# Optimization experiments

Hardware: AMD Instinct MI355X
Metric: run time of the kernel (lower is better)

## Reference

```python
import jax, jax.numpy as jnp
import numpy as np

B, T_V, T_A = 128, 64, 128
E_V, E_A = 1024, 512
H, EMB, C = 1024, 512, 512  # C = input_size - embedding_size
IN = EMB + C               # RNN input size = 1024
VOCAB = 20000


def setup_inputs() -> dict:
    key = jax.random.key(0)
    ks = jax.random.split(key, 26)
    s = 0.02
    inp = {
        "input": jax.random.normal(ks[0], (B, 1, EMB), jnp.float32),
        "enc_visual": jax.random.normal(ks[1], (B, T_V, E_V), jnp.float32),
        "enc_audio": jax.random.normal(ks[2], (B, T_A, E_A), jnp.float32),
        "hidden_state": jax.random.normal(ks[3], (1, B, H), jnp.float32),
        "cell_state": jax.random.normal(ks[4], (1, B, H), jnp.float32),
        # visual attention (Bahdanau): W1:[C,H], W2:[C,E_V], W3:[1,C]
        "W_va1": s * jax.random.normal(ks[5], (C, H), jnp.float32),
        "W_va2": s * jax.random.normal(ks[6], (C, E_V), jnp.float32),
        "W_va3": s * jax.random.normal(ks[7], (1, C), jnp.float32),
        "W_venc": s * jax.random.normal(ks[8], (C, E_V), jnp.float32),
        # audio attention
        "W_aa1": s * jax.random.normal(ks[9], (C, H), jnp.float32),
        "W_aa2": s * jax.random.normal(ks[10], (C, E_A), jnp.float32),
        "W_aa3": s * jax.random.normal(ks[11], (1, C), jnp.float32),
        "W_aenc": s * jax.random.normal(ks[12], (C, E_A), jnp.float32),
        # cross-modal context attention (over 2 context vectors)
        "W_ca1": s * jax.random.normal(ks[13], (C, H), jnp.float32),
        "W_ca2": s * jax.random.normal(ks[14], (C, C), jnp.float32),
        "W_ca3": s * jax.random.normal(ks[15], (1, C), jnp.float32),
        # LSTM-style custom RNN cell params
        "W_ih": s * jax.random.normal(ks[16], (4 * H, IN), jnp.float32),
        "W_hh": s * jax.random.normal(ks[17], (4 * H, H), jnp.float32),
        "b_ih": jnp.zeros((4 * H,), jnp.float32),
        "b_hh": jnp.zeros((4 * H,), jnp.float32),
        # output projection
        "W_out": s * jax.random.normal(ks[18], (VOCAB, H), jnp.float32),
        "b_out": jnp.zeros((VOCAB,), jnp.float32),
    }
    return inp


def _attend(h, enc, W1, W2, W3):
    # h: [B,H]; enc: [B,T,E]. Vectorized Bahdanau attention (original loops over T).
    v1 = h @ W1.T                               # [B,C]
    v2 = jnp.einsum('bte,ce->btc', enc, W2)     # [B,T,C]
    scores = jnp.tanh(v1[:, None, :] + v2) @ W3.T  # [B,T,1]
    attn = jax.nn.softmax(scores[..., 0], axis=1)  # [B,T]
    return jnp.einsum('bt,bte->be', attn, enc)     # [B,E]


def reference(input, enc_visual, enc_audio, hidden_state, cell_state,
              W_va1, W_va2, W_va3, W_venc,
              W_aa1, W_aa2, W_aa3, W_aenc,
              W_ca1, W_ca2, W_ca3,
              W_ih, W_hh, b_ih, b_hh, W_out, b_out):
    h0 = hidden_state[0]   # [B,H]
    c0 = cell_state[0]     # [B,H]

    vc = _attend(h0, enc_visual, W_va1, W_va2, W_va3) @ W_venc.T  # [B,C]
    ac = _attend(h0, enc_audio, W_aa1, W_aa2, W_aa3) @ W_aenc.T   # [B,C]
    all_ctx = jnp.stack([vc, ac], axis=1)                         # [B,2,C]
    final_ctx = _attend(h0, all_ctx, W_ca1, W_ca2, W_ca3)         # [B,C]

    x = jnp.concatenate([input[:, 0, :], jnp.tanh(final_ctx)], axis=-1)  # [B,IN]
    gates = x @ W_ih.T + b_ih + h0 @ W_hh.T + b_hh                 # [B,4H]
    i, f, g, o = jnp.split(gates, 4, axis=-1)
    c_new = jax.nn.sigmoid(f) * c0 + jax.nn.sigmoid(i) * jnp.tanh(g)
    h_new = jax.nn.sigmoid(o) * jnp.tanh(c_new)

    logits = h_new @ W_out.T + b_out                               # [B,V]
    return (logits[:, None, :], h_new[None], c_new[None])
```

## Files before the change

kernel.cpp:

```cpp
#include <hip/hip_runtime.h>
#include <hip/hip_bf16.h>
#include <cstddef>

typedef __attribute__((ext_vector_type(8))) short short8;
typedef __attribute__((ext_vector_type(4))) float f32x4;

#define LSTR 40

static __device__ __forceinline__ short8 pack8(float4 f0, float4 f1) {
    union { __hip_bfloat162 h[4]; short8 s; } u;
    u.h[0] = __float22bfloat162_rn(make_float2(f0.x, f0.y));
    u.h[1] = __float22bfloat162_rn(make_float2(f0.z, f0.w));
    u.h[2] = __float22bfloat162_rn(make_float2(f1.x, f1.y));
    u.h[3] = __float22bfloat162_rn(make_float2(f1.z, f1.w));
    return u.s;
}

static __device__ __forceinline__ void sk_body(
    const float* __restrict__ A, int lda,
    const float* __restrict__ W,
    const float* __restrict__ bias, int addbias,
    float* __restrict__ C, int ldc, int N,
    int kbeg, int kend, int n0, int m0)
{
    __shared__ short As[128 * LSTR];
    __shared__ short Ws[64 * LSTR];
    const int tid  = threadIdx.x;
    const int lane = tid & 63;
    const int wave = tid >> 6;
    const int wm = wave * 32;

    f32x4 acc[2][4];
    #pragma unroll
    for (int i = 0; i < 2; ++i)
        #pragma unroll
        for (int j = 0; j < 4; ++j)
            acc[i][j] = (f32x4){0.f, 0.f, 0.f, 0.f};

    const int srow  = tid >> 2;
    const int skoff = (tid & 3) * 8;
    const int frow  = lane & 15;
    const int fkoff = (lane >> 4) * 8;

    for (int k0 = kbeg; k0 < kend; k0 += 32) {
        #pragma unroll
        for (int p = 0; p < 2; ++p) {
            int row = srow + p * 64;
            const float* sa = A + (size_t)(m0 + row) * lda + k0 + skoff;
            *(short8*)(As + row * LSTR + skoff) =
                pack8(*(const float4*)sa, *(const float4*)(sa + 4));
        }
        {
            int n = n0 + srow;
            short8 v = (short8){0,0,0,0,0,0,0,0};
            if (n < N) {
                const float* sw = W + (size_t)n * lda + k0 + skoff;
                v = pack8(*(const float4*)sw, *(const float4*)(sw + 4));
            }
            *(short8*)(Ws + srow * LSTR + skoff) = v;
        }
        __syncthreads();

        short8 af[2], bf[4];
        #pragma unroll
        for (int i = 0; i < 2; ++i)
            af[i] = *(const short8*)(As + (wm + i * 16 + frow) * LSTR + fkoff);
        #pragma unroll
        for (int j = 0; j < 4; ++j)
            bf[j] = *(const short8*)(Ws + (j * 16 + frow) * LSTR + fkoff);
        #pragma unroll
        for (int i = 0; i < 2; ++i)
            #pragma unroll
            for (int j = 0; j < 4; ++j)
                acc[i][j] = __builtin_amdgcn_mfma_f32_16x16x32_bf16(af[i], bf[j], acc[i][j], 0, 0, 0);
        __syncthreads();
    }

    const int cl = lane & 15;
    const int rq = (lane >> 4) * 4;
    #pragma unroll
    for (int j = 0; j < 4; ++j) {
        int gc = n0 + j * 16 + cl;
        if (gc >= N) continue;
        float b = addbias ? bias[gc] : 0.f;
        #pragma unroll
        for (int i = 0; i < 2; ++i) {
            int gr = m0 + wm + i * 16 + rq;
            #pragma unroll
            for (int r = 0; r < 4; ++r)
                atomicAdd(C + (size_t)(gr + r) * ldc + gc, acc[i][j][r] + b);
        }
    }
}

__global__ __launch_bounds__(256) void gemm_sk(
    const float* __restrict__ A, const float* __restrict__ W,
    const float* __restrict__ bias, float* __restrict__ C,
    int N, int K, int kchunk, int ldc)
{
    int kbeg = blockIdx.y * kchunk;
    sk_body(A, K, W, bias, bias != nullptr && blockIdx.y == 0,
            C, ldc, N, kbeg, kbeg + kchunk, blockIdx.x * 64, blockIdx.z * 128);
}

__global__ __launch_bounds__(256) void hproj3_mfma(
    const float* __restrict__ h0,
    const float* __restrict__ Wa, const float* __restrict__ Wb, const float* __restrict__ Wc,
    float* __restrict__ hbase)
{
    int n0g = blockIdx.x * 64;
    int wsel = n0g >> 9;
    const float* W = (wsel == 0) ? Wa : (wsel == 1) ? Wb : Wc;
    float* C = hbase + (size_t)wsel * 128 * 512;
    int kbeg = blockIdx.y * 128;
    sk_body(h0, 1024, W, nullptr, 0, C, 512, 512, kbeg, kbeg + 128, n0g & 511, 0);
}

__global__ __launch_bounds__(256) void ctxproj_mfma(
    const float* __restrict__ attv, const float* __restrict__ Wv,
    const float* __restrict__ atta, const float* __restrict__ Wa,
    float* __restrict__ ctx)
{
    const float* A; const float* W; float* C; int lda, kb, ke;
    if (blockIdx.z == 0) { A = attv; W = Wv; C = ctx;       lda = 1024; kb = blockIdx.y * 128; ke = kb + 128; }
    else                 { A = atta; W = Wa; C = ctx + 512; lda = 512;  kb = blockIdx.y * 64;  ke = kb + 64;  }
    sk_body(A, lda, W, nullptr, 0, C, 1024, 512, kb, ke, blockIdx.x * 64, 0);
}

__global__ __launch_bounds__(256) void gates_mfma(
    const float* __restrict__ xb, const float* __restrict__ W_ih,
    const float* __restrict__ h0, const float* __restrict__ W_hh,
    float* __restrict__ gates)
{
    int pair = blockIdx.y >> 2;
    const float* A = pair ? h0 : xb;
    const float* W = pair ? W_hh : W_ih;
    int kb = (blockIdx.y & 3) * 256;
    sk_body(A, 1024, W, nullptr, 0, gates, 4096, 4096, kb, kb + 256, blockIdx.x * 64, 0);
}

__global__ __launch_bounds__(256) void scores_fused(
    const float* __restrict__ encv, const float* __restrict__ W_va2,
    const float* __restrict__ hv1,  const float* __restrict__ W_va3,
    float* __restrict__ scv,
    const float* __restrict__ enca, const float* __restrict__ W_aa2,
    const float* __restrict__ ha1,  const float* __restrict__ W_aa3,
    float* __restrict__ sca)
{
    __shared__ short As[64 * LSTR];
    __shared__ short Ws[128 * LSTR];

    const float *A, *W, *v1, *W3;
    float* sc;
    int K, tshift, n0, m0;
    int idx = blockIdx.x;
    if (idx < 512) {
        n0 = (idx >> 7) * 128;  m0 = (idx & 127) * 64;
        A = encv; W = W_va2; v1 = hv1; W3 = W_va3; sc = scv;
        K = 1024; tshift = 6;
    } else {
        idx -= 512;
        n0 = (idx >> 8) * 128;  m0 = (idx & 255) * 64;
        A = enca; W = W_aa2; v1 = ha1; W3 = W_aa3; sc = sca;
        K = 512; tshift = 7;
    }

    const int tid  = threadIdx.x;
    const int lane = tid & 63;
    const int wave = tid >> 6;
    const int wm = (wave >> 1) * 32;
    const int wn = (wave & 1) * 64;

    f32x4 acc[2][4];
    #pragma unroll
    for (int i = 0; i < 2; ++i)
        #pragma unroll
        for (int j = 0; j < 4; ++j)
            acc[i][j] = (f32x4){0.f, 0.f, 0.f, 0.f};

    const int srow  = tid >> 2;
    const int skoff = (tid & 3) * 8;
    const int frow  = lane & 15;
    const int fkoff = (lane >> 4) * 8;

    for (int k0 = 0; k0 < K; k0 += 32) {
        {
            const float* sa = A + (size_t)(m0 + srow) * K + k0 + skoff;
            *(short8*)(As + srow * LSTR + skoff) =
                pack8(*(const float4*)sa, *(const float4*)(sa + 4));
        }
        #pragma unroll
        for (int p = 0; p < 2; ++p) {
            int row = srow + p * 64;
            const float* sw = W + (size_t)(n0 + row) * K + k0 + skoff;
            *(short8*)(Ws + row * LSTR + skoff) =
                pack8(*(const float4*)sw, *(const float4*)(sw + 4));
        }
        __syncthreads();

        short8 af[2], bf[4];
        #pragma unroll
        for (int i = 0; i < 2; ++i)
            af[i] = *(const short8*)(As + (wm + i * 16 + frow) * LSTR + fkoff);
        #pragma unroll
        for (int j = 0; j < 4; ++j)
            bf[j] = *(const short8*)(Ws + (wn + j * 16 + frow) * LSTR + fkoff);
        #pragma unroll
        for (int i = 0; i < 2; ++i)
            #pragma unroll
            for (int j = 0; j < 4; ++j)
                acc[i][j] = __builtin_amdgcn_mfma_f32_16x16x32_bf16(af[i], bf[j], acc[i][j], 0, 0, 0);
        __syncthreads();
    }

    const int cl = lane & 15;
    const int rq = (lane >> 4) * 4;
    #pragma unroll
    for (int i = 0; i < 2; ++i) {
        #pragma unroll
        for (int r = 0; r < 4; ++r) {
            int gr = m0 + wm + i * 16 + rq + r;
            const float* v1row = v1 + (size_t)(gr >> tshift) * 512;
            float p = 0.f;
            #pragma unroll
            for (int j = 0; j < 4; ++j) {
                int gc = n0 + wn + j * 16 + cl;
                p += tanhf(v1row[gc] + acc[i][j][r]) * W3[gc];
            }
            p += __shfl_xor(p, 1, 64);
            p += __shfl_xor(p, 2, 64);
            p += __shfl_xor(p, 4, 64);
            p += __shfl_xor(p, 8, 64);
            if (cl == 0) atomicAdd(sc + gr, p);
        }
    }
}

__global__ __launch_bounds__(256) void attend_out2(
    const float* __restrict__ scv, const float* __restrict__ encv, float* __restrict__ attv,
    const float* __restrict__ sca, const float* __restrict__ enca, float* __restrict__ atta)
{
    const float* sc; const float* enc; float* out;
    int T, E, ec;
    if (blockIdx.y < 4) { sc = scv; enc = encv; out = attv; T = 64;  E = 1024; ec = blockIdx.y; }
    else                { sc = sca; enc = enca; out = atta; T = 128; E = 512;  ec = blockIdx.y - 4; }

    __shared__ float ew[128];
    const int b = blockIdx.x, tid = threadIdx.x;
    __shared__ float raw[128];
    if (tid < T) raw[tid] = sc[(size_t)b * T + tid];
    __syncthreads();
    float m = -1e30f;
    for (int t = 0; t < T; ++t) m = fmaxf(m, raw[t]);
    if (tid < T) ew[tid] = __expf(raw[tid] - m);
    __syncthreads();
    float sum = 0.f;
    for (int t = 0; t < T; ++t) sum += ew[t];
    const float inv = 1.f / sum;

    const int e = ec * 256 + tid;
    const float* encb = enc + (size_t)b * T * E + e;
    float acc = 0.f;
    for (int t = 0; t < T; ++t)
        acc += ew[t] * encb[(size_t)t * E];
    out[(size_t)b * E + e] = acc * inv;
}

__global__ __launch_bounds__(256) void cross_kernel(
    const float* __restrict__ hc1, const float* __restrict__ v2c,
    const float* __restrict__ W3, const float* __restrict__ ctx,
    const float* __restrict__ inp, float* __restrict__ x)
{
    const int C = 512;
    __shared__ float red[256];
    __shared__ float aw[2];
    const int b = blockIdx.x, tid = threadIdx.x;

    float p0 = 0.f, p1 = 0.f;
    for (int c = tid; c < C; c += 256) {
        float h = hc1[(size_t)b * C + c], w = W3[c];
        p0 += tanhf(h + v2c[(size_t)(b * 2 + 0) * C + c]) * w;
        p1 += tanhf(h + v2c[(size_t)(b * 2 + 1) * C + c]) * w;
    }
    red[tid] = p0; __syncthreads();
    for (int s = 128; s; s >>= 1) { if (tid < s) red[tid] += red[tid + s]; __syncthreads(); }
    float s0 = red[0];
    __syncthreads();
    red[tid] = p1; __syncthreads();
    for (int s = 128; s; s >>= 1) { if (tid < s) red[tid] += red[tid + s]; __syncthreads(); }
    if (tid == 0) {
        float s1 = red[0];
        float m = fmaxf(s0, s1);
        float e0 = __expf(s0 - m), e1 = __expf(s1 - m);
        float inv = 1.f / (e0 + e1);
        aw[0] = e0 * inv; aw[1] = e1 * inv;
    }
    __syncthreads();
    float a0 = aw[0], a1 = aw[1];
    for (int c = tid; c < C; c += 256) {
        float fc = a0 * ctx[(size_t)(b * 2 + 0) * C + c]
                 + a1 * ctx[(size_t)(b * 2 + 1) * C + c];
        x[(size_t)b * 1024 + 512 + c] = tanhf(fc);
        x[(size_t)b * 1024 + c] = inp[(size_t)b * 512 + c];
    }
}

__global__ __launch_bounds__(256) void lstm_kernel(
    const float* __restrict__ gates, const float* __restrict__ c0,
    const float* __restrict__ b_ih, const float* __restrict__ b_hh,
    float* __restrict__ hout, float* __restrict__ cout)
{
    const int idx = blockIdx.x * 256 + threadIdx.x;
    const int b = idx >> 10, h = idx & 1023;
    const float* g = gates + (size_t)b * 4096;
    float gi = g[h]        + b_ih[h]        + b_hh[h];
    float gf = g[1024 + h] + b_ih[1024 + h] + b_hh[1024 + h];
    float gg = g[2048 + h] + b_ih[2048 + h] + b_hh[2048 + h];
    float go = g[3072 + h] + b_ih[3072 + h] + b_hh[3072 + h];
    float si = 1.f / (1.f + __expf(-gi));
    float sf = 1.f / (1.f + __expf(-gf));
    float so = 1.f / (1.f + __expf(-go));
    float cn = sf * c0[idx] + si * tanhf(gg);
    float hn = so * tanhf(cn);
    cout[idx] = cn;
    hout[idx] = hn;
}

extern "C" void kernel_launch(void* const* d_in, const int* in_sizes, int n_in,
                              void* d_out, int out_size, void* d_ws, size_t ws_size,
                              hipStream_t stream)
{
    const float* inp    = (const float*)d_in[0];
    const float* encv   = (const float*)d_in[1];
    const float* enca   = (const float*)d_in[2];
    const float* h0     = (const float*)d_in[3];
    const float* c0     = (const float*)d_in[4];
    const float* W_va1  = (const float*)d_in[5];
    const float* W_va2  = (const float*)d_in[6];
    const float* W_va3  = (const float*)d_in[7];
    const float* W_venc = (const float*)d_in[8];
    const float* W_aa1  = (const float*)d_in[9];
    const float* W_aa2  = (const float*)d_in[10];
    const float* W_aa3  = (const float*)d_in[11];
    const float* W_aenc = (const float*)d_in[12];
    const float* W_ca1  = (const float*)d_in[13];
    const float* W_ca2  = (const float*)d_in[14];
    const float* W_ca3  = (const float*)d_in[15];
    const float* W_ih   = (const float*)d_in[16];
    const float* W_hh   = (const float*)d_in[17];
    const float* b_ih   = (const float*)d_in[18];
    const float* b_hh   = (const float*)d_in[19];
    const float* W_out  = (const float*)d_in[20];
    const float* b_out  = (const float*)d_in[21];
    float* out = (float*)d_out;

    float* ws = (float*)d_ws;
    float* hv1  = ws;  ws += 128 * 512;
    float* ha1  = ws;  ws += 128 * 512;
    float* hc1  = ws;  ws += 128 * 512;
    float* scv  = ws;  ws += 128 * 64;
    float* sca  = ws;  ws += 128 * 128;
    float* ctx  = ws;  ws += 128 * 2 * 512;
    float* v2c  = ws;  ws += 128 * 2 * 512;
    float* gates= ws;  ws += (size_t)128 * 4096;
    size_t zero_floats = (size_t)(ws - (float*)d_ws);
    float* xb   = ws;  ws += 128 * 1024;
    float* attv = ws;  ws += 128 * 1024;
    float* atta = ws;  ws += 128 * 512;

    dim3 blk(256);

    hipMemsetAsync(d_ws, 0, zero_floats * sizeof(float), stream);
    hipMemsetAsync(out, 0, (size_t)128 * 20000 * sizeof(float), stream);

    hproj3_mfma<<<dim3(24, 8), blk, 0, stream>>>(h0, W_va1, W_aa1, W_ca1, hv1);
    scores_fused<<<dim3(1536), blk, 0, stream>>>(encv, W_va2, hv1, W_va3, scv,
                                                 enca, W_aa2, ha1, W_aa3, sca);
    attend_out2<<<dim3(128, 6), blk, 0, stream>>>(scv, encv, attv, sca, enca, atta);
    ctxproj_mfma<<<dim3(8, 8, 2), blk, 0, stream>>>(attv, W_venc, atta, W_aenc, ctx);
    gemm_sk<<<dim3(8, 4, 2), blk, 0, stream>>>(ctx, W_ca2, nullptr, v2c, 512, 512, 128, 512);
    cross_kernel<<<128, blk, 0, stream>>>(hc1, v2c, W_ca3, ctx, inp, xb);
    gates_mfma<<<dim3(64, 8), blk, 0, stream>>>(xb, W_ih, h0, W_hh, gates);
    float* hout = out + 2560000;
    float* cout = out + 2560000 + 131072;
    lstm_kernel<<<512, blk, 0, stream>>>(gates, c0, b_ih, b_hh, hout, cout);
    gemm_sk<<<dim3(313, 2, 1), blk, 0, stream>>>(hout, W_out, b_out, out, 20000, 1024, 512, 20000);
}
```

Baseline: 398.5 us.

## Enlarge scores GEMM tile to 128x128, prefetch globals, swizzle LDS

The fused attention-score GEMM now uses 128x128 tiles instead of 64x128, which halves the block count and doubles per-wave MFMA work for more operand reuse. Global loads for the next K-slice go into registers while the current slice is computed, so global latency overlaps with compute. The padded LDS layout is replaced by an XOR-swizzled 32-wide layout meant to avoid bank conflicts without padding. The cost is higher register pressure (more accumulators plus prefetch buffers) and fewer blocks, which may lower occupancy.

```diff
diff --git a/kernel.cpp b/kernel.cpp
--- a/kernel.cpp
+++ b/kernel.cpp
@@ -147,20 +147,20 @@
     const float* __restrict__ ha1,  const float* __restrict__ W_aa3,
     float* __restrict__ sca)
 {
-    __shared__ short As[64 * LSTR];
-    __shared__ short Ws[128 * LSTR];
+    __shared__ short As[128 * 32];
+    __shared__ short Ws[128 * 32];
 
     const float *A, *W, *v1, *W3;
     float* sc;
     int K, tshift, n0, m0;
     int idx = blockIdx.x;
-    if (idx < 512) {
-        n0 = (idx >> 7) * 128;  m0 = (idx & 127) * 64;
+    if (idx < 256) {
+        n0 = (idx >> 6) * 128;  m0 = (idx & 63) * 128;
         A = encv; W = W_va2; v1 = hv1; W3 = W_va3; sc = scv;
         K = 1024; tshift = 6;
     } else {
-        idx -= 512;
-        n0 = (idx >> 8) * 128;  m0 = (idx & 255) * 64;
+        idx -= 256;
+        n0 = (idx >> 7) * 128;  m0 = (idx & 127) * 128;
         A = enca; W = W_aa2; v1 = ha1; W3 = W_aa3; sc = sca;
         K = 512; tshift = 7;
     }
@@ -168,45 +168,63 @@
     const int tid  = threadIdx.x;
     const int lane = tid & 63;
     const int wave = tid >> 6;
-    const int wm = (wave >> 1) * 32;
+    const int wm = (wave >> 1) * 64;
     const int wn = (wave & 1) * 64;
 
-    f32x4 acc[2][4];
+    f32x4 acc[4][4];
     #pragma unroll
-    for (int i = 0; i < 2; ++i)
+    for (int i = 0; i < 4; ++i)
         #pragma unroll
         for (int j = 0; j < 4; ++j)
             acc[i][j] = (f32x4){0.f, 0.f, 0.f, 0.f};
 
-    const int srow  = tid >> 2;
-    const int skoff = (tid & 3) * 8;
+    const int srow = tid >> 1;
+    const int skh  = tid & 1;
+    const float* ga = A + (size_t)(m0 + srow) * K + skh * 16;
+    const float* gw = W + (size_t)(n0 + srow) * K + skh * 16;
+    const int fs = (srow >> 1) & 3;
+    short* wa0 = As + srow * 32 + (((skh * 2)     ^ fs) * 8);
+    short* wa1 = As + srow * 32 + (((skh * 2 + 1) ^ fs) * 8);
+    short* ww0 = Ws + srow * 32 + (((skh * 2)     ^ fs) * 8);
+    short* ww1 = Ws + srow * 32 + (((skh * 2 + 1) ^ fs) * 8);
+
     const int frow  = lane & 15;
-    const int fkoff = (lane >> 4) * 8;
+    const int hi    = lane >> 4;
+    const int fslot = (hi ^ ((frow >> 1) & 3)) * 8;
+    const short* ra = As + (wm + frow) * 32 + fslot;
+    const short* rb = Ws + (wn + frow) * 32 + fslot;
+
+    float4 pa[4], pw[4];
+    #pragma unroll
+    for (int q = 0; q < 4; ++q) {
+        pa[q] = *(const float4*)(ga + q * 4);
+        pw[q] = *(const float4*)(gw + q * 4);
+    }
 
     for (int k0 = 0; k0 < K; k0 += 32) {
-        {
-            const float* sa = A + (size_t)(m0 + srow) * K + k0 + skoff;
-            *(short8*)(As + srow * LSTR + skoff) =
-                pack8(*(const float4*)sa, *(const float4*)(sa + 4));
+        *(short8*)wa0 = pack8(pa[0], pa[1]);
+        *(short8*)wa1 = pack8(pa[2], pa[3]);
+        *(short8*)ww0 = pack8(pw[0], pw[1]);
+        *(short8*)ww1 = pack8(pw[2], pw[3]);
+        __syncthreads();
+
+        if (k0 + 32 < K) {
+            #pragma unroll
+            for (int q = 0; q < 4; ++q) {
+                pa[q] = *(const float4*)(ga + k0 + 32 + q * 4);
+                pw[q] = *(const float4*)(gw + k0 + 32 + q * 4);
+            }
         }
-        #pragma unroll
-        for (int p = 0; p < 2; ++p) {
-            int row = srow + p * 64;
-            const float* sw = W + (size_t)(n0 + row) * K + k0 + skoff;
-            *(short8*)(Ws + row * LSTR + skoff) =
-                pack8(*(const float4*)sw, *(const float4*)(sw + 4));
-        }
-        __syncthreads();
-
-        short8 af[2], bf[4];
-        #pragma unroll
-        for (int i = 0; i < 2; ++i)
-            af[i] = *(const short8*)(As + (wm + i * 16 + frow) * LSTR + fkoff);
+
+        short8 af[4], bf[4];
+        #pragma unroll
+        for (int i = 0; i < 4; ++i)
+            af[i] = *(const short8*)(ra + i * 512);
         #pragma unroll
         for (int j = 0; j < 4; ++j)
-            bf[j] = *(const short8*)(Ws + (wn + j * 16 + frow) * LSTR + fkoff);
-        #pragma unroll
-        for (int i = 0; i < 2; ++i)
+            bf[j] = *(const short8*)(rb + j * 512);
+        #pragma unroll
+        for (int i = 0; i < 4; ++i)
             #pragma unroll
             for (int j = 0; j < 4; ++j)
                 acc[i][j] = __builtin_amdgcn_mfma_f32_16x16x32_bf16(af[i], bf[j], acc[i][j], 0, 0, 0);
@@ -214,9 +232,9 @@
     }
 
     const int cl = lane & 15;
-    const int rq = (lane >> 4) * 4;
+    const int rq = hi * 4;
     #pragma unroll
-    for (int i = 0; i < 2; ++i) {
+    for (int i = 0; i < 4; ++i) {
         #pragma unroll
         for (int r = 0; r < 4; ++r) {
             int gr = m0 + wm + i * 16 + rq + r;
@@ -374,8 +392,8 @@
     hipMemsetAsync(out, 0, (size_t)128 * 20000 * sizeof(float), stream);
 
     hproj3_mfma<<<dim3(24, 8), blk, 0, stream>>>(h0, W_va1, W_aa1, W_ca1, hv1);
-    scores_fused<<<dim3(1536), blk, 0, stream>>>(encv, W_va2, hv1, W_va3, scv,
-                                                 enca, W_aa2, ha1, W_aa3, sca);
+    scores_fused<<<dim3(768), blk, 0, stream>>>(encv, W_va2, hv1, W_va3, scv,
+                                                enca, W_aa2, ha1, W_aa3, sca);
     attend_out2<<<dim3(128, 6), blk, 0, stream>>>(scv, encv, attv, sca, enca, atta);
     ctxproj_mfma<<<dim3(8, 8, 2), blk, 0, stream>>>(attv, W_venc, atta, W_aenc, ctx);
     gemm_sk<<<dim3(8, 4, 2), blk, 0, stream>>>(ctx, W_ca2, nullptr, v2c, 512, 512, 128, 512);
```

Result: slower. 412.7 us (+3.6%).

## Double-buffer LDS tiles with register prefetch and XOR-swizzled layout in GEMMs

Applied to the files above, without the earlier changes.

Both the split-K GEMM body and the fused attention-score GEMM now prefetch the next K-slice from global memory into registers while the current slice is consumed from LDS. They use two LDS buffers so the trailing barrier can be dropped. The padded LDS stride is replaced by an unpadded 32-element row with an XOR swizzle, meant to avoid bank conflicts without wasting space. This targets global-load latency stalls and one barrier per iteration, at the cost of doubled LDS use and more live registers.

```diff
diff --git a/kernel.cpp b/kernel.cpp
--- a/kernel.cpp
+++ b/kernel.cpp
@@ -4,8 +4,6 @@
 
 typedef __attribute__((ext_vector_type(8))) short short8;
 typedef __attribute__((ext_vector_type(4))) float f32x4;
-
-#define LSTR 40
 
 static __device__ __forceinline__ short8 pack8(float4 f0, float4 f1) {
     union { __hip_bfloat162 h[4]; short8 s; } u;
@@ -23,8 +21,8 @@
     float* __restrict__ C, int ldc, int N,
     int kbeg, int kend, int n0, int m0)
 {
-    __shared__ short As[128 * LSTR];
-    __shared__ short Ws[64 * LSTR];
+    __shared__ short As[2][128 * 32];
+    __shared__ short Ws[2][64 * 32];
     const int tid  = threadIdx.x;
     const int lane = tid & 63;
     const int wave = tid >> 6;
@@ -37,47 +35,64 @@
         for (int j = 0; j < 4; ++j)
             acc[i][j] = (f32x4){0.f, 0.f, 0.f, 0.f};
 
-    const int srow  = tid >> 2;
-    const int skoff = (tid & 3) * 8;
-    const int frow  = lane & 15;
-    const int fkoff = (lane >> 4) * 8;
-
-    for (int k0 = kbeg; k0 < kend; k0 += 32) {
-        #pragma unroll
-        for (int p = 0; p < 2; ++p) {
-            int row = srow + p * 64;
-            const float* sa = A + (size_t)(m0 + row) * lda + k0 + skoff;
-            *(short8*)(As + row * LSTR + skoff) =
-                pack8(*(const float4*)sa, *(const float4*)(sa + 4));
-        }
-        {
-            int n = n0 + srow;
-            short8 v = (short8){0,0,0,0,0,0,0,0};
-            if (n < N) {
-                const float* sw = W + (size_t)n * lda + k0 + skoff;
-                v = pack8(*(const float4*)sw, *(const float4*)(sw + 4));
+    const int arow = tid >> 1;
+    const int ah   = tid & 1;
+    const int afs  = (arow >> 1) & 3;
+    const float* gA = A + (size_t)(m0 + arow) * lda + kbeg + ah * 16;
+    const int aoff0 = arow * 32 + (((ah * 2)     ^ afs) * 8);
+    const int aoff1 = arow * 32 + (((ah * 2 + 1) ^ afs) * 8);
+
+    const int wrow  = tid >> 2;
+    const int wslot = tid & 3;
+    const int wvalid = (n0 + wrow) < N;
+    const float* gW = W + (size_t)(n0 + wrow) * lda + kbeg + wslot * 8;
+    const int woff = wrow * 32 + ((wslot ^ ((wrow >> 1) & 3)) * 8);
+
+    const int frow = lane & 15;
+    const int hi   = lane >> 4;
+    const int fsl  = (hi ^ ((frow >> 1) & 3)) * 8;
+    const int ra   = (wm + frow) * 32 + fsl;
+    const int rb   = frow * 32 + fsl;
+
+    float4 pa0, pa1, pa2, pa3, pw0, pw1;
+    pa0 = *(const float4*)(gA);      pa1 = *(const float4*)(gA + 4);
+    pa2 = *(const float4*)(gA + 8);  pa3 = *(const float4*)(gA + 12);
+    if (wvalid) { pw0 = *(const float4*)(gW); pw1 = *(const float4*)(gW + 4); }
+    else        { pw0 = make_float4(0,0,0,0); pw1 = make_float4(0,0,0,0); }
+
+    const int nsteps = (kend - kbeg) >> 5;
+    for (int s = 0; s < nsteps; ++s) {
+        short* as = As[s & 1];
+        short* ws = Ws[s & 1];
+        *(short8*)(as + aoff0) = pack8(pa0, pa1);
+        *(short8*)(as + aoff1) = pack8(pa2, pa3);
+        *(short8*)(ws + woff)  = pack8(pw0, pw1);
+        if (s + 1 < nsteps) {
+            const float* nA = gA + (s + 1) * 32;
+            pa0 = *(const float4*)(nA);      pa1 = *(const float4*)(nA + 4);
+            pa2 = *(const float4*)(nA + 8);  pa3 = *(const float4*)(nA + 12);
+            if (wvalid) {
+                const float* nW = gW + (s + 1) * 32;
+                pw0 = *(const float4*)(nW); pw1 = *(const float4*)(nW + 4);
             }
-            *(short8*)(Ws + srow * LSTR + skoff) = v;
         }
         __syncthreads();
-
         short8 af[2], bf[4];
         #pragma unroll
         for (int i = 0; i < 2; ++i)
-            af[i] = *(const short8*)(As + (wm + i * 16 + frow) * LSTR + fkoff);
+            af[i] = *(const short8*)(as + ra + i * 512);
         #pragma unroll
         for (int j = 0; j < 4; ++j)
-            bf[j] = *(const short8*)(Ws + (j * 16 + frow) * LSTR + fkoff);
+            bf[j] = *(const short8*)(ws + rb + j * 512);
         #pragma unroll
         for (int i = 0; i < 2; ++i)
             #pragma unroll
             for (int j = 0; j < 4; ++j)
                 acc[i][j] = __builtin_amdgcn_mfma_f32_16x16x32_bf16(af[i], bf[j], acc[i][j], 0, 0, 0);
-        __syncthreads();
     }
 
     const int cl = lane & 15;
-    const int rq = (lane >> 4) * 4;
+    const int rq = hi * 4;
     #pragma unroll
     for (int j = 0; j < 4; ++j) {
         int gc = n0 + j * 16 + cl;
@@ -147,8 +162,8 @@
     const float* __restrict__ ha1,  const float* __restrict__ W_aa3,
     float* __restrict__ sca)
 {
-    __shared__ short As[64 * LSTR];
-    __shared__ short Ws[128 * LSTR];
+    __shared__ short As[2][64 * 32];
+    __shared__ short Ws[2][128 * 32];
 
     const float *A, *W, *v1, *W3;
     float* sc;
@@ -178,43 +193,60 @@
         for (int j = 0; j < 4; ++j)
             acc[i][j] = (f32x4){0.f, 0.f, 0.f, 0.f};
 
-    const int srow  = tid >> 2;
-    const int skoff = (tid & 3) * 8;
-    const int frow  = lane & 15;
-    const int fkoff = (lane >> 4) * 8;
-
-    for (int k0 = 0; k0 < K; k0 += 32) {
-        {
-            const float* sa = A + (size_t)(m0 + srow) * K + k0 + skoff;
-            *(short8*)(As + srow * LSTR + skoff) =
-                pack8(*(const float4*)sa, *(const float4*)(sa + 4));
-        }
-        #pragma unroll
-        for (int p = 0; p < 2; ++p) {
-            int row = srow + p * 64;
-            const float* sw = W + (size_t)(n0 + row) * K + k0 + skoff;
-            *(short8*)(Ws + row * LSTR + skoff) =
-                pack8(*(const float4*)sw, *(const float4*)(sw + 4));
+    const int arow  = tid >> 2;
+    const int aslot = tid & 3;
+    const float* gA = A + (size_t)(m0 + arow) * K + aslot * 8;
+    const int aoff  = arow * 32 + ((aslot ^ ((arow >> 1) & 3)) * 8);
+
+    const int wrow = tid >> 1;
+    const int wh   = tid & 1;
+    const int wfs  = (wrow >> 1) & 3;
+    const float* gW = W + (size_t)(n0 + wrow) * K + wh * 16;
+    const int woff0 = wrow * 32 + (((wh * 2)     ^ wfs) * 8);
+    const int woff1 = wrow * 32 + (((wh * 2 + 1) ^ wfs) * 8);
+
+    const int frow = lane & 15;
+    const int hi   = lane >> 4;
+    const int fsl  = (hi ^ ((frow >> 1) & 3)) * 8;
+    const int ra   = (wm + frow) * 32 + fsl;
+    const int rb   = (wn + frow) * 32 + fsl;
+
+    float4 pa0, pa1, pw0, pw1, pw2, pw3;
+    pa0 = *(const float4*)(gA);      pa1 = *(const float4*)(gA + 4);
+    pw0 = *(const float4*)(gW);      pw1 = *(const float4*)(gW + 4);
+    pw2 = *(const float4*)(gW + 8);  pw3 = *(const float4*)(gW + 12);
+
+    const int nsteps = K >> 5;
+    for (int s = 0; s < nsteps; ++s) {
+        short* as = As[s & 1];
+        short* ws = Ws[s & 1];
+        *(short8*)(as + aoff)  = pack8(pa0, pa1);
+        *(short8*)(ws + woff0) = pack8(pw0, pw1);
+        *(short8*)(ws + woff1) = pack8(pw2, pw3);
+        if (s + 1 < nsteps) {
+            const float* nA = gA + (s + 1) * 32;
+            pa0 = *(const float4*)(nA);      pa1 = *(const float4*)(nA + 4);
+            const float* nW = gW + (s + 1) * 32;
+            pw0 = *(const float4*)(nW);      pw1 = *(const float4*)(nW + 4);
+            pw2 = *(const float4*)(nW + 8);  pw3 = *(const float4*)(nW + 12);
         }
         __syncthreads();
-
         short8 af[2], bf[4];
         #pragma unroll
         for (int i = 0; i < 2; ++i)
-            af[i] = *(const short8*)(As + (wm + i * 16 + frow) * LSTR + fkoff);
+            af[i] = *(const short8*)(as + ra + i * 512);
         #pragma unroll
         for (int j = 0; j < 4; ++j)
-            bf[j] = *(const short8*)(Ws + (wn + j * 16 + frow) * LSTR + fkoff);
+            bf[j] = *(const short8*)(ws + rb + j * 512);
         #pragma unroll
         for (int i = 0; i < 2; ++i)
             #pragma unroll
             for (int j = 0; j < 4; ++j)
                 acc[i][j] = __builtin_amdgcn_mfma_f32_16x16x32_bf16(af[i], bf[j], acc[i][j], 0, 0, 0);
-        __syncthreads();
     }
 
     const int cl = lane & 15;
-    const int rq = (lane >> 4) * 4;
+    const int rq = hi * 4;
     #pragma unroll
     for (int i = 0; i < 2; ++i) {
         #pragma unroll
```

Measured after the change: 388.2 us. 2.6% less time.
